# Optimization experiments

Hardware: AMD Instinct MI355X
Metric: run time of the kernel (lower is better)

The kernel has to match this reference:

```python
import jax, jax.numpy as jnp
import numpy as np

NUM_HEADS = 12
SEG_HEADS = 6  # first 6 heads -> full attention; rest -> 4-way strided
HEAD_DIM = 64


def setup_inputs() -> dict:
    key = jax.random.key(0)
    ks = jax.random.split(key, 7)
    B, S, H = 2, 4096, 768
    sc = 0.02
    return {
        "hidden_states": jax.random.normal(ks[0], (B, S, H), jnp.float32),
        "Wq": jax.random.normal(ks[1], (H, H), jnp.float32) * sc,
        "bq": jax.random.normal(ks[2], (H,), jnp.float32) * sc,
        "Wk": jax.random.normal(ks[3], (H, H), jnp.float32) * sc,
        "bk": jax.random.normal(ks[4], (H,), jnp.float32) * sc,
        "Wv": jax.random.normal(ks[5], (H, H), jnp.float32) * sc,
        "bv": jax.random.normal(ks[6], (H,), jnp.float32) * sc,
    }


def _heads(x, B, S):
    # [B,S,H] -> [B,nH,S,D]
    return x.reshape(B, S, NUM_HEADS, HEAD_DIM).transpose(0, 2, 1, 3)


def reference(hidden_states, Wq, bq, Wk, bk, Wv, bv):
    B, S, H = hidden_states.shape
    scale = 1.0 / jnp.sqrt(jnp.float32(HEAD_DIM))

    q = _heads(hidden_states @ Wq.T + bq, B, S)
    k = _heads(hidden_states @ Wk.T + bk, B, S)
    v = _heads(hidden_states @ Wv.T + bv, B, S)

    # ---- full attention on first SEG_HEADS heads ----
    qf, kf, vf = q[:, :SEG_HEADS], k[:, :SEG_HEADS], v[:, :SEG_HEADS]
    scores = jnp.einsum('bhqd,bhkd->bhqk', qf, kf) * scale
    z_full = jnp.einsum('bhqk,bhkd->bhqd', jax.nn.softmax(scores, axis=-1), vf)

    # ---- 4-way strided attention on remaining heads ----
    # x[:,:,i::4,:] == reshape(B,h,S//4,4,D)[..., i, :]; batch the 4 groups.
    S4 = S // 4
    def strided(x):
        # [B,h,S,D] -> [B,h,4,S//4,D], group g holds positions g::4
        return x[:, SEG_HEADS:].reshape(B, NUM_HEADS - SEG_HEADS, S4, 4, HEAD_DIM).transpose(0, 1, 3, 2, 4)
    qa, ka, va = strided(q), strided(k), strided(v)
    s_ax = jnp.einsum('bhgqd,bhgkd->bhgqk', qa, ka) * scale
    z_ax = jnp.einsum('bhgqk,bhgkd->bhgqd', jax.nn.softmax(s_ax, axis=-1), va)
    # re-interleave: torch.stack(dim=3).view -> position s*4+g from (g,s)
    z_axis = z_ax.transpose(0, 1, 3, 2, 4).reshape(B, NUM_HEADS - SEG_HEADS, S, HEAD_DIM)

    ctx = jnp.concatenate([z_full, z_axis], axis=1)           # [B,nH,S,D]
    ctx = ctx.transpose(0, 2, 1, 3).reshape(B, S, NUM_HEADS * HEAD_DIM)
    return ctx
```

## Files before the change

### kernel.cpp

```cpp
#include <hip/hip_runtime.h>
#include <stdint.h>
#include <math.h>

#define BB 2
#define SS 4096
#define NHEADS 12
#define DHEAD 64

#define N_HS (8192*768)
#define N_W  (768*768)

typedef __bf16 bf16x8 __attribute__((ext_vector_type(8)));
typedef float  f32x4  __attribute__((ext_vector_type(4)));
typedef float  f32x16 __attribute__((ext_vector_type(16)));

__device__ __forceinline__ unsigned short f2bf(float x) {
  union { float f; uint32_t u; } v; v.f = x;
  uint32_t r = v.u + 0x7fffu + ((v.u >> 16) & 1u);
  return (unsigned short)(r >> 16);
}

__device__ __forceinline__ float fexp2(float x) {
#if __has_builtin(__builtin_amdgcn_exp2f)
  return __builtin_amdgcn_exp2f(x);
#else
  return exp2f(x);
#endif
}

__device__ __forceinline__ unsigned int pk_trunc(float lo, float hi) {
#if __has_builtin(__builtin_amdgcn_perm)
  return __builtin_amdgcn_perm(__float_as_uint(hi), __float_as_uint(lo), 0x07060302u);
#else
  return (__float_as_uint(hi) & 0xffff0000u) | (__float_as_uint(lo) >> 16);
#endif
}

__device__ __forceinline__ void gld16(const unsigned short* g, unsigned short* l) {
  __builtin_amdgcn_global_load_lds(
      (const __attribute__((address_space(1))) unsigned int*)g,
      (__attribute__((address_space(3))) unsigned int*)l, 16, 0, 0);
}

__global__ __launch_bounds__(256) void convert_kernel(
    const float* __restrict__ hs, const float* __restrict__ wq,
    const float* __restrict__ wk, const float* __restrict__ wv,
    unsigned short* __restrict__ hs_bf, unsigned short* __restrict__ w_bf)
{
  int i = blockIdx.x * 256 + threadIdx.x;
  const int total4 = (N_HS + 3 * N_W) / 4;
  if (i >= total4) return;
  int e = i * 4;
  const float* src; int rel; unsigned short* dst; int dofs;
  if (e < N_HS) { src = hs; rel = e; dst = hs_bf; dofs = e; }
  else {
    int r = e - N_HS; dst = w_bf; dofs = r;
    if      (r < N_W)     { src = wq; rel = r; }
    else if (r < 2 * N_W) { src = wk; rel = r - N_W; }
    else                  { src = wv; rel = r - 2 * N_W; }
  }
  float4 v = *(const float4*)(src + rel);
  union { unsigned short s[4]; uint2 u; } o;
  o.s[0] = f2bf(v.x); o.s[1] = f2bf(v.y); o.s[2] = f2bf(v.z); o.s[3] = f2bf(v.w);
  *(uint2*)(dst + dofs) = o.u;
}

__global__ __launch_bounds__(256) void qkv_gemm(
    const unsigned short* __restrict__ hs,
    const unsigned short* __restrict__ w_all,
    const float* __restrict__ bq, const float* __restrict__ bk, const float* __restrict__ bv,
    unsigned short* __restrict__ qh,
    unsigned short* __restrict__ kh,
    unsigned short* __restrict__ vt)
{
  __shared__ __align__(16) unsigned short SM[2 * 128 * 64];
  unsigned short* At = SM;
  unsigned short* Bt = SM + 128 * 64;

  const int bid = blockIdx.x;
  const int xcd = bid & 7;
  const int t   = bid >> 3;
  const int st  = (t / 48) * 8 + xcd;
  const int inner = t % 48;
  const int which = st >> 3;
  const int mbase = (st & 7) * 1024 + (inner & 7) * 128;
  const int nb    = (inner >> 3) * 128;

  const int tid = threadIdx.x;
  const unsigned short* w = w_all + (size_t)which * (768 * 768);
  const int lane = tid & 63, wid = tid >> 6;
  const int ln = lane & 15, qd = lane >> 4;
  const int wm = wid >> 1, wn = wid & 1;

  const int srow = lane >> 3;
  const int sslot = (lane & 7) ^ srow;

  f32x4 acc[4][4];
#pragma unroll
  for (int i = 0; i < 4; i++)
#pragma unroll
    for (int j = 0; j < 4; j++) acc[i][j] = (f32x4){0.f, 0.f, 0.f, 0.f};

  for (int kb = 0; kb < 12; ++kb) {
    const int kbase = kb * 64;
    __syncthreads();
#pragma unroll
    for (int j = 0; j < 4; ++j) {
      int c = wid * 4 + j;
      int row = c * 8 + srow;
      gld16(hs + (size_t)(mbase + row) * 768 + kbase + sslot * 8, &At[c * 512]);
      gld16(w  + (size_t)(nb    + row) * 768 + kbase + sslot * 8, &Bt[c * 512]);
    }
    __syncthreads();
#pragma unroll
    for (int ks = 0; ks < 2; ++ks) {
      bf16x8 af[4], bfr[4];
#pragma unroll
      for (int t2 = 0; t2 < 4; t2++) {
        int ra = wm * 64 + t2 * 16 + ln;
        int rb = wn * 64 + t2 * 16 + ln;
        int slot = (qd + 4 * ks);
        af[t2]  = *(const bf16x8*)(&At[ra * 64 + ((slot ^ (ra & 7)) * 8)]);
        bfr[t2] = *(const bf16x8*)(&Bt[rb * 64 + ((slot ^ (rb & 7)) * 8)]);
      }
#pragma unroll
      for (int i = 0; i < 4; i++)
#pragma unroll
        for (int j = 0; j < 4; j++)
          acc[i][j] = __builtin_amdgcn_mfma_f32_16x16x32_bf16(af[i], bfr[j], acc[i][j], 0, 0, 0);
    }
  }

  const float* bias = (which == 0) ? bq : (which == 1) ? bk : bv;
  const float postscale = (which == 0) ? 0.18033688011112042f : 1.0f;
  const int n0 = nb + wn * 64;
  const int hh = n0 >> 6;
  const int mrow0 = mbase + wm * 64;
  const int bgl = mrow0 >> 12;
  const int s0 = mrow0 & 4095;
  const bool axisv = (which == 2) && (hh >= 6);

  __syncthreads();
  unsigned short* T = SM + wid * 4096;

  if (which < 2) {
#pragma unroll
    for (int j = 0; j < 4; j++) {
      float bb = bias[n0 + j * 16 + ln];
#pragma unroll
      for (int i = 0; i < 4; i++)
#pragma unroll
        for (int r = 0; r < 4; r++)
          T[(i * 16 + qd * 4 + r) * 64 + j * 16 + ln] =
              f2bf((acc[i][j][r] + bb) * postscale);
    }
  } else if (!axisv) {
#pragma unroll
    for (int j = 0; j < 4; j++) {
      float bb = bias[n0 + j * 16 + ln];
#pragma unroll
      for (int i = 0; i < 4; i++) {
        unsigned int p01 = (unsigned int)f2bf(acc[i][j][0] + bb) |
                           ((unsigned int)f2bf(acc[i][j][1] + bb) << 16);
        unsigned int p23 = (unsigned int)f2bf(acc[i][j][2] + bb) |
                           ((unsigned int)f2bf(acc[i][j][3] + bb) << 16);
        int base = (j * 16 + ln) * 64 + i * 16 + qd * 4;
        *(unsigned int*)(&T[base])     = p01;
        *(unsigned int*)(&T[base + 2]) = p23;
      }
    }
  } else {
#pragma unroll
    for (int j = 0; j < 4; j++) {
      float bb = bias[n0 + j * 16 + ln];
#pragma unroll
      for (int i = 0; i < 4; i++)
#pragma unroll
        for (int r = 0; r < 4; r++)
          T[(j * 16 + ln) * 64 + r * 16 + i * 4 + qd] = f2bf(acc[i][j][r] + bb);
    }
  }
  __syncthreads();

  if (which < 2) {
    unsigned short* dp = ((which == 0) ? qh : kh) +
                         ((size_t)(bgl * 12 + hh) * 4096 + s0) * 64;
#pragma unroll
    for (int c = 0; c < 8; ++c) {
      int lin = c * 64 + lane;
      int row = lin >> 3, sl8 = (lin & 7) * 8;
      *(uint4*)(dp + row * 64 + sl8) = *(const uint4*)(&T[row * 64 + sl8]);
    }
  } else if (!axisv) {
    unsigned short* dp = vt + (size_t)(bgl * 12 + hh) * 64 * 4096 + s0;
#pragma unroll
    for (int c = 0; c < 8; ++c) {
      int lin = c * 64 + lane;
      int drow = lin >> 3, sl8 = (lin & 7) * 8;
      *(uint4*)(dp + (size_t)drow * 4096 + sl8) = *(const uint4*)(&T[drow * 64 + sl8]);
    }
  } else {
    const int i0_0 = s0 >> 2;
    unsigned short* dp = vt + (size_t)(bgl * 12 + hh) * 64 * 4096;
#pragma unroll
    for (int c = 0; c < 8; ++c) {
      int lin = c * 64 + lane;
      int drow = lin >> 3, sl = lin & 7;
      int g = sl >> 1, io = (sl & 1) * 8;
      *(uint4*)(dp + (size_t)drow * 4096 + g * 1024 + i0_0 + io) =
          *(const uint4*)(&T[drow * 64 + sl * 8]);
    }
  }
}

__device__ __forceinline__ void make_frags(const unsigned int* P, int hi,
                                           bf16x8* fa, bf16x8* fb) {
  unsigned int s0 = hi ? P[0] : P[2];
  unsigned int s1 = hi ? P[1] : P[3];
  unsigned int r0 = (unsigned int)__shfl_xor((int)s0, 32, 64);
  unsigned int r1 = (unsigned int)__shfl_xor((int)s1, 32, 64);
  unsigned int t0 = hi ? P[4] : P[6];
  unsigned int t1 = hi ? P[5] : P[7];
  unsigned int u0 = (unsigned int)__shfl_xor((int)t0, 32, 64);
  unsigned int u1 = (unsigned int)__shfl_xor((int)t1, 32, 64);
  union { unsigned int u[4]; bf16x8 v; } A, B;
  A.u[0] = hi ? r0 : P[0];
  A.u[1] = hi ? r1 : P[1];
  A.u[2] = hi ? P[2] : r0;
  A.u[3] = hi ? P[3] : r1;
  B.u[0] = hi ? u0 : P[4];
  B.u[1] = hi ? u1 : P[5];
  B.u[2] = hi ? P[6] : u0;
  B.u[3] = hi ? P[7] : u1;
  *fa = A.v; *fb = B.v;
}

__global__ __launch_bounds__(256, 2) void attn_kernel(
    const unsigned short* __restrict__ qh,
    const unsigned short* __restrict__ kh,
    const unsigned short* __restrict__ vt,
    float* __restrict__ out,
    float* __restrict__ PO, float* __restrict__ PL)
{
  __shared__ __align__(16) unsigned short Kt[2 * 64 * 72];
  __shared__ __align__(16) unsigned short Vt[2 * 64 * 72];

  const int bid = blockIdx.x;
  int b, h, g, qt, nkt, kt0, strided, half, bh;
  if (bid < 384) {
    int xcd = bid & 7, t = bid >> 3;
    int gb = t >> 4; qt = t & 15;
    int gfull = gb * 8 + xcd;
    bh = gfull >> 1; half = gfull & 1;
    b = bh / 6; h = bh % 6;
    g = 0; strided = 0; nkt = 32; kt0 = half * 32;
  } else {
    int r = bid - 384;
    int xcd = r & 7, t = r >> 3;
    int gb = t >> 2; qt = t & 3;
    int g2 = gb * 8 + xcd;
    int bhi = g2 >> 2; g = g2 & 3;
    b = bhi / 6; h = 6 + bhi % 6;
    strided = 1; nkt = 16; kt0 = 0; half = 0; bh = 0;
  }
  const size_t headoff = (size_t)(b * 12 + h) * 4096 * 64;
  const unsigned short* qp = qh + headoff;
  const unsigned short* kp = kh + headoff;
  const unsigned short* vp = vt + headoff;

  const int tid = threadIdx.x;
  const int lane = tid & 63, w = tid >> 6;
  const int l32 = lane & 31, hi = lane >> 5;
  const int hi8 = hi * 8;

  const int qrowA = qt * 256 + w * 64 + l32;
  const int sQA = strided ? (qrowA * 4 + g) : qrowA;
  const int sQB = sQA + (strided ? 128 : 32);
  bf16x8 qfA[4], qfB[4];
#pragma unroll
  for (int c = 0; c < 4; ++c) {
    qfA[c] = *(const bf16x8*)(qp + (size_t)sQA * 64 + c * 16 + hi8);
    qfB[c] = *(const bf16x8*)(qp + (size_t)sQB * 64 + c * 16 + hi8);
  }

  union { unsigned int u[4]; bf16x8 v; } ones_;
#pragma unroll
  for (int i = 0; i < 4; i++) ones_.u[i] = 0x3f803f80u;
  const bf16x8 onesf = ones_.v;

  const int srow0 = tid >> 3,        scol0 = (tid & 7) * 8;
  const int srow1 = (tid + 256) >> 3, scol1 = ((tid + 256) & 7) * 8;
  const int s0g = kt0 * 64 + srow0, s1g = kt0 * 64 + srow1;
  const unsigned short* kptr0 = kp + (size_t)(strided ? (s0g * 4 + g) : s0g) * 64 + scol0;
  const unsigned short* kptr1 = kp + (size_t)(strided ? (s1g * 4 + g) : s1g) * 64 + scol1;
  const int vb0 = strided ? g * 1024 : 0;
  const unsigned short* vptr0 = vp + (size_t)srow0 * 4096 + vb0 + kt0 * 64 + scol0;
  const unsigned short* vptr1 = vp + (size_t)srow1 * 4096 + vb0 + kt0 * 64 + scol1;
  const int kstep = (strided ? 256 : 64) * 64;
  const int lofs0 = srow0 * 72 + scol0, lofs1 = srow1 * 72 + scol1;

  uint4 rk0 = *(const uint4*)kptr0, rk1 = *(const uint4*)kptr1;
  uint4 rv0 = *(const uint4*)vptr0, rv1 = *(const uint4*)vptr1;
  kptr0 += kstep; kptr1 += kstep; vptr0 += 64; vptr1 += 64;
  *(uint4*)(&Kt[lofs0]) = rk0; *(uint4*)(&Kt[lofs1]) = rk1;
  *(uint4*)(&Vt[lofs0]) = rv0; *(uint4*)(&Vt[lofs1]) = rv1;
  __syncthreads();

  f32x16 oA0, oA1, oB0, oB1, laccA, laccB;
#pragma unroll
  for (int i = 0; i < 16; i++) {
    oA0[i] = 0.f; oA1[i] = 0.f; oB0[i] = 0.f; oB1[i] = 0.f;
    laccA[i] = 0.f; laccB[i] = 0.f;
  }

  for (int kt = 0; kt < nkt; ++kt) {
    const int cur = (kt & 1) * 4608, nxt = 4608 - cur;
    const bool pf = (kt + 1 < nkt);
    if (pf) {
      rk0 = *(const uint4*)kptr0; rk1 = *(const uint4*)kptr1;
      rv0 = *(const uint4*)vptr0; rv1 = *(const uint4*)vptr1;
      kptr0 += kstep; kptr1 += kstep; vptr0 += 64; vptr1 += 64;
    }

    f32x16 scA0, scA1, scB0, scB1;
#pragma unroll
    for (int i = 0; i < 16; i++) { scA0[i] = 0.f; scA1[i] = 0.f; scB0[i] = 0.f; scB1[i] = 0.f; }
#pragma unroll
    for (int c = 0; c < 4; ++c) {
      bf16x8 k0 = *(const bf16x8*)(&Kt[cur + l32 * 72 + c * 16 + hi8]);
      bf16x8 k1 = *(const bf16x8*)(&Kt[cur + (32 + l32) * 72 + c * 16 + hi8]);
      scA0 = __builtin_amdgcn_mfma_f32_32x32x16_bf16(k0, qfA[c], scA0, 0, 0, 0);
      scA1 = __builtin_amdgcn_mfma_f32_32x32x16_bf16(k1, qfA[c], scA1, 0, 0, 0);
      scB0 = __builtin_amdgcn_mfma_f32_32x32x16_bf16(k0, qfB[c], scB0, 0, 0, 0);
      scB1 = __builtin_amdgcn_mfma_f32_32x32x16_bf16(k1, qfB[c], scB1, 0, 0, 0);
    }

    bf16x8 pfrA[4], pfrB[4];
    {
      unsigned int P0[8], P1[8];
#pragma unroll
      for (int u = 0; u < 8; ++u) {
        P0[u] = pk_trunc(fexp2(scA0[2 * u]), fexp2(scA0[2 * u + 1]));
        P1[u] = pk_trunc(fexp2(scA1[2 * u]), fexp2(scA1[2 * u + 1]));
      }
      make_frags(P0, hi, &pfrA[0], &pfrA[1]);
      make_frags(P1, hi, &pfrA[2], &pfrA[3]);
    }
    {
      unsigned int P0[8], P1[8];
#pragma unroll
      for (int u = 0; u < 8; ++u) {
        P0[u] = pk_trunc(fexp2(scB0[2 * u]), fexp2(scB0[2 * u + 1]));
        P1[u] = pk_trunc(fexp2(scB1[2 * u]), fexp2(scB1[2 * u + 1]));
      }
      make_frags(P0, hi, &pfrB[0], &pfrB[1]);
      make_frags(P1, hi, &pfrB[2], &pfrB[3]);
    }

#pragma unroll
    for (int c = 0; c < 4; ++c) {
      bf16x8 v0 = *(const bf16x8*)(&Vt[cur + l32 * 72 + c * 16 + hi8]);
      bf16x8 v1 = *(const bf16x8*)(&Vt[cur + (32 + l32) * 72 + c * 16 + hi8]);
      oA0 = __builtin_amdgcn_mfma_f32_32x32x16_bf16(v0, pfrA[c], oA0, 0, 0, 0);
      oA1 = __builtin_amdgcn_mfma_f32_32x32x16_bf16(v1, pfrA[c], oA1, 0, 0, 0);
      oB0 = __builtin_amdgcn_mfma_f32_32x32x16_bf16(v0, pfrB[c], oB0, 0, 0, 0);
      oB1 = __builtin_amdgcn_mfma_f32_32x32x16_bf16(v1, pfrB[c], oB1, 0, 0, 0);
      laccA = __builtin_amdgcn_mfma_f32_32x32x16_bf16(onesf, pfrA[c], laccA, 0, 0, 0);
      laccB = __builtin_amdgcn_mfma_f32_32x32x16_bf16(onesf, pfrB[c], laccB, 0, 0, 0);
    }

    if (pf) {
      *(uint4*)(&Kt[nxt + lofs0]) = rk0; *(uint4*)(&Kt[nxt + lofs1]) = rk1;
      *(uint4*)(&Vt[nxt + lofs0]) = rv0; *(uint4*)(&Vt[nxt + lofs1]) = rv1;
    }
    __syncthreads();
  }

  const float ltotA = laccA[0], ltotB = laccB[0];
  if (!strided) {
    size_t baseA = ((size_t)(bh * 2 + half) * 4096 + sQA) * 64;
    size_t baseB = ((size_t)(bh * 2 + half) * 4096 + sQB) * 64;
#pragma unroll
    for (int mt = 0; mt < 2; ++mt) {
#pragma unroll
      for (int a = 0; a < 4; ++a) {
        float4 va, vb;
        va.x = mt ? oA1[4 * a + 0] : oA0[4 * a + 0];
        va.y = mt ? oA1[4 * a + 1] : oA0[4 * a + 1];
        va.z = mt ? oA1[4 * a + 2] : oA0[4 * a + 2];
        va.w = mt ? oA1[4 * a + 3] : oA0[4 * a + 3];
        vb.x = mt ? oB1[4 * a + 0] : oB0[4 * a + 0];
        vb.y = mt ? oB1[4 * a + 1] : oB0[4 * a + 1];
        vb.z = mt ? oB1[4 * a + 2] : oB0[4 * a + 2];
        vb.w = mt ? oB1[4 * a + 3] : oB0[4 * a + 3];
        *(float4*)(&PO[baseA + mt * 32 + a * 8 + hi * 4]) = va;
        *(float4*)(&PO[baseB + mt * 32 + a * 8 + hi * 4]) = vb;
      }
    }
    if (hi == 0) {
      PL[(bh * 2 + half) * 4096 + sQA] = ltotA;
      PL[(bh * 2 + half) * 4096 + sQB] = ltotB;
    }
  } else {
    float invA = 1.0f / ltotA, invB = 1.0f / ltotB;
    size_t baseA = ((size_t)b * 4096 + sQA) * 768 + h * 64;
    size_t baseB = ((size_t)b * 4096 + sQB) * 768 + h * 64;
#pragma unroll
    for (int mt = 0; mt < 2; ++mt) {
#pragma unroll
      for (int a = 0; a < 4; ++a) {
        float4 va, vb;
        va.x = (mt ? oA1[4 * a + 0] : oA0[4 * a + 0]) * invA;
        va.y = (mt ? oA1[4 * a + 1] : oA0[4 * a + 1]) * invA;
        va.z = (mt ? oA1[4 * a + 2] : oA0[4 * a + 2]) * invA;
        va.w = (mt ? oA1[4 * a + 3] : oA0[4 * a + 3]) * invA;
        vb.x = (mt ? oB1[4 * a + 0] : oB0[4 * a + 0]) * invB;
        vb.y = (mt ? oB1[4 * a + 1] : oB0[4 * a + 1]) * invB;
        vb.z = (mt ? oB1[4 * a + 2] : oB0[4 * a + 2]) * invB;
        vb.w = (mt ? oB1[4 * a + 3] : oB0[4 * a + 3]) * invB;
        *(float4*)(&out[baseA + mt * 32 + a * 8 + hi * 4]) = va;
        *(float4*)(&out[baseB + mt * 32 + a * 8 + hi * 4]) = vb;
      }
    }
  }
}

__global__ __launch_bounds__(256) void merge_kernel(
    const float* __restrict__ PO, const float* __restrict__ PL,
    float* __restrict__ out)
{
  int i = blockIdx.x * 256 + threadIdx.x;
  int c4 = i & 15;
  int qrow = (i >> 4) & 4095;
  int bh = i >> 16;
  size_t p0 = (((size_t)bh * 2 + 0) * 4096 + qrow) * 64 + c4 * 4;
  size_t p1 = (((size_t)bh * 2 + 1) * 4096 + qrow) * 64 + c4 * 4;
  float4 a = *(const float4*)(&PO[p0]);
  float4 c = *(const float4*)(&PO[p1]);
  float l = PL[(bh * 2 + 0) * 4096 + qrow] + PL[(bh * 2 + 1) * 4096 + qrow];
  float inv = 1.0f / l;
  float4 o;
  o.x = (a.x + c.x) * inv; o.y = (a.y + c.y) * inv;
  o.z = (a.z + c.z) * inv; o.w = (a.w + c.w) * inv;
  int b = bh / 6, h = bh % 6;
  *(float4*)(&out[((size_t)b * 4096 + qrow) * 768 + h * 64 + c4 * 4]) = o;
}

extern "C" void kernel_launch(void* const* d_in, const int* in_sizes, int n_in,
                              void* d_out, int out_size, void* d_ws, size_t ws_size,
                              hipStream_t stream) {
  const float* hs = (const float*)d_in[0];
  const float* Wq = (const float*)d_in[1];
  const float* bq = (const float*)d_in[2];
  const float* Wk = (const float*)d_in[3];
  const float* bk = (const float*)d_in[4];
  const float* Wv = (const float*)d_in[5];
  const float* bv = (const float*)d_in[6];
  float* out = (float*)d_out;

  unsigned short* q_bf  = (unsigned short*)d_ws;
  unsigned short* k_bf  = q_bf + (size_t)BB * NHEADS * SS * DHEAD;
  unsigned short* vt_bf = k_bf + (size_t)BB * NHEADS * SS * DHEAD;
  unsigned short* hs_bf = vt_bf + (size_t)BB * NHEADS * SS * DHEAD;
  unsigned short* w_bf  = hs_bf + (size_t)N_HS;
  float* PO = (float*)hs_bf;
  float* PL = PO + (size_t)12 * 2 * 4096 * 64;

  const int total4 = (N_HS + 3 * N_W) / 4;
  convert_kernel<<<(total4 + 255) / 256, 256, 0, stream>>>(hs, Wq, Wk, Wv, hs_bf, w_bf);

  qkv_gemm<<<1152, 256, 0, stream>>>(hs_bf, w_bf, bq, bk, bv, q_bf, k_bf, vt_bf);

  attn_kernel<<<576, 256, 0, stream>>>(q_bf, k_bf, vt_bf, out, PO, PL);

  merge_kernel<<<3072, 256, 0, stream>>>(PO, PL, out);
}
```

Before: 225.4 us.

## Double-buffer QKV GEMM tiles with register prefetch instead of direct LDS loads

```diff
diff --git a/kernel.cpp b/kernel.cpp
--- a/kernel.cpp
+++ b/kernel.cpp
@@ -34,12 +34,6 @@
 #else
   return (__float_as_uint(hi) & 0xffff0000u) | (__float_as_uint(lo) >> 16);
 #endif
-}
-
-__device__ __forceinline__ void gld16(const unsigned short* g, unsigned short* l) {
-  __builtin_amdgcn_global_load_lds(
-      (const __attribute__((address_space(1))) unsigned int*)g,
-      (__attribute__((address_space(3))) unsigned int*)l, 16, 0, 0);
 }
 
 __global__ __launch_bounds__(256) void convert_kernel(
@@ -73,9 +67,7 @@
     unsigned short* __restrict__ kh,
     unsigned short* __restrict__ vt)
 {
-  __shared__ __align__(16) unsigned short SM[2 * 128 * 64];
-  unsigned short* At = SM;
-  unsigned short* Bt = SM + 128 * 64;
+  __shared__ __align__(16) unsigned short SM[4 * 128 * 64];
 
   const int bid = blockIdx.x;
   const int xcd = bid & 7;
@@ -95,23 +87,46 @@
   const int srow = lane >> 3;
   const int sslot = (lane & 7) ^ srow;
 
+  const unsigned short* gA[4];
+  const unsigned short* gB[4];
+#pragma unroll
+  for (int j = 0; j < 4; ++j) {
+    int row = (wid * 4 + j) * 8 + srow;
+    gA[j] = hs + (size_t)(mbase + row) * 768 + sslot * 8;
+    gB[j] = w  + (size_t)(nb    + row) * 768 + sslot * 8;
+  }
+  const int ldofs = (tid >> 6) * 0;
+
   f32x4 acc[4][4];
 #pragma unroll
   for (int i = 0; i < 4; i++)
 #pragma unroll
     for (int j = 0; j < 4; j++) acc[i][j] = (f32x4){0.f, 0.f, 0.f, 0.f};
 
+  uint4 pa[4], pb[4];
+#pragma unroll
+  for (int j = 0; j < 4; ++j) { pa[j] = *(const uint4*)gA[j]; pb[j] = *(const uint4*)gB[j]; }
+#pragma unroll
+  for (int j = 0; j < 4; ++j) {
+    int c = wid * 4 + j;
+    *(uint4*)(&SM[c * 512 + lane * 8])        = pa[j];
+    *(uint4*)(&SM[8192 + c * 512 + lane * 8]) = pb[j];
+  }
+  __syncthreads();
+
   for (int kb = 0; kb < 12; ++kb) {
-    const int kbase = kb * 64;
-    __syncthreads();
-#pragma unroll
-    for (int j = 0; j < 4; ++j) {
-      int c = wid * 4 + j;
-      int row = c * 8 + srow;
-      gld16(hs + (size_t)(mbase + row) * 768 + kbase + sslot * 8, &At[c * 512]);
-      gld16(w  + (size_t)(nb    + row) * 768 + kbase + sslot * 8, &Bt[c * 512]);
-    }
-    __syncthreads();
+    const int cur = (kb & 1) * 16384;
+    const bool pf = (kb + 1 < 12);
+    if (pf) {
+      const int kbase = (kb + 1) * 64;
+#pragma unroll
+      for (int j = 0; j < 4; ++j) {
+        pa[j] = *(const uint4*)(gA[j] + kbase);
+        pb[j] = *(const uint4*)(gB[j] + kbase);
+      }
+    }
+    const unsigned short* At = SM + cur;
+    const unsigned short* Bt = SM + cur + 8192;
 #pragma unroll
     for (int ks = 0; ks < 2; ++ks) {
       bf16x8 af[4], bfr[4];
@@ -129,6 +144,16 @@
         for (int j = 0; j < 4; j++)
           acc[i][j] = __builtin_amdgcn_mfma_f32_16x16x32_bf16(af[i], bfr[j], acc[i][j], 0, 0, 0);
     }
+    if (pf) {
+      const int nxt = 16384 - cur;
+#pragma unroll
+      for (int j = 0; j < 4; ++j) {
+        int c = wid * 4 + j;
+        *(uint4*)(&SM[nxt + c * 512 + lane * 8])        = pa[j];
+        *(uint4*)(&SM[nxt + 8192 + c * 512 + lane * 8]) = pb[j];
+      }
+    }
+    __syncthreads();
   }
 
   const float* bias = (which == 0) ? bq : (which == 1) ? bk : bv;
@@ -140,7 +165,6 @@
   const int s0 = mrow0 & 4095;
   const bool axisv = (which == 2) && (hh >= 6);
 
-  __syncthreads();
   unsigned short* T = SM + wid * 4096;
 
   if (which < 2) {
```

New measurement: 230.1 us. +2.1%, slower.
